# Performance work log

Hardware: AMD Instinct MI355X
Metric: run time of the kernel (lower is better)

Reference implementation:

```python
import jax, jax.numpy as jnp
import numpy as np

B, CIN, COUT, K, L = 16, 512, 512, 3, 8192
STRIDE, PAD, DIL = 1, 1, 1  # 'same' conv: Lout == L


def setup_inputs() -> dict:
    key = jax.random.key(0)
    k1, k2, k3 = jax.random.split(key, 3)
    x = jax.random.normal(k1, (B, CIN, L), dtype=jnp.float32)
    # int8 quantized weight stored as int32 for portability; values in [-128, 127]
    qweight = jax.random.randint(k2, (COUT, CIN, K), -128, 128, dtype=jnp.int32)
    scale = jnp.float32(0.01)  # per-tensor dequant scale (w_max / 127)
    bias = jax.random.normal(k3, (COUT,), dtype=jnp.float32)
    return {"x": x, "qweight": qweight, "scale": scale, "bias": bias}


def reference(x, qweight, scale, bias):
    # Dequantize: fp32 weight = int8 * scale (materialized every call, as in torch module)
    w = (qweight.astype(jnp.float32) * scale).astype(x.dtype)
    out = jax.lax.conv_general_dilated(
        x, w,
        window_strides=(STRIDE,),
        padding=[(PAD, PAD)],
        rhs_dilation=(DIL,),
        dimension_numbers=("NCH", "OIH", "NCH"),
        feature_group_count=1,
    )
    return out + bias.astype(x.dtype)[None, :, None]
```

## Files before the change

kernel.cpp:

```cpp
#include <hip/hip_runtime.h>
#include <hip/hip_bf16.h>

#define CIN   512
#define COUT  512
#define LEN   8192
#define NB    16
#define KW    3
#define PROWS 8200

#define WB_ELEMS (COUT * CIN * KW)
#define WB_BYTES ((size_t)WB_ELEMS * 2)
#define XS_BYTES ((size_t)NB * PROWS * CIN * 2)

#define BM2 256
#define BN2 256
#define BK3 64
#define NT  ((CIN / BK3) * KW)
#define TILE3 (BM2 * BK3 * 2)

typedef __attribute__((ext_vector_type(4))) float f32x4;
typedef __attribute__((ext_vector_type(8))) short bf16x8;

static __device__ __forceinline__ unsigned short f2bf(float f) {
    union { float f; unsigned u; } cv; cv.f = f;
    return (unsigned short)((cv.u + 0x7fffu + ((cv.u >> 16) & 1u)) >> 16);
}

__global__ __launch_bounds__(256) void wconv_kernel(const int* __restrict__ q,
                                                    unsigned short* __restrict__ wb) {
    int idx = blockIdx.x * 256 + threadIdx.x;
    if (idx >= WB_ELEMS) return;
    int co = idx / (KW * CIN);
    int r  = idx - co * (KW * CIN);
    int t  = r >> 9;
    int ci = r & 511;
    wb[idx] = f2bf((float)q[(co * CIN + ci) * KW + t]);
}

__global__ __launch_bounds__(256) void xprep_kernel(const float* __restrict__ x,
                                                    unsigned short* __restrict__ xs) {
    __shared__ char T[64 * 132];
    int blk = blockIdx.x;
    int b   = blk >> 10;
    int ci0 = ((blk >> 7) & 7) * 64;
    int l0  = (blk & 127) * 64;
    int tid = threadIdx.x;

    if (l0 == 0 && tid < 64)
        xs[((size_t)b * PROWS + 0) * CIN + ci0 + tid] = 0;
    if (l0 == (LEN - 64) && tid < 64)
        xs[((size_t)b * PROWS + (LEN + 1)) * CIN + ci0 + tid] = 0;

    const float* src = x + ((size_t)b * CIN + ci0) * LEN + l0;
    for (int i = tid; i < 64 * 16; i += 256) {
        int r = i >> 4, c4 = i & 15;
        f32x4 v = *(const f32x4*)(src + (size_t)r * LEN + c4 * 4);
        unsigned lo = (unsigned)f2bf(v[0]) | ((unsigned)f2bf(v[1]) << 16);
        unsigned hi = (unsigned)f2bf(v[2]) | ((unsigned)f2bf(v[3]) << 16);
        char* p = T + r * 132 + c4 * 8;
        *(unsigned*)p       = lo;
        *(unsigned*)(p + 4) = hi;
    }
    __syncthreads();
    unsigned short* dst = xs + ((size_t)b * PROWS + 1 + l0) * CIN + ci0;
    for (int i = tid; i < 64 * 8; i += 256) {
        int l = i >> 3, c8 = i & 7;
        union { bf16x8 v; unsigned short s[8]; } pk;
        #pragma unroll
        for (int j = 0; j < 8; ++j)
            pk.s[j] = *(const unsigned short*)(T + (c8 * 8 + j) * 132 + l * 2);
        *(bf16x8*)(dst + (size_t)l * CIN + c8 * 8) = pk.v;
    }
}

__global__ __launch_bounds__(512, 2) void conv_kernel(
    const unsigned short* __restrict__ xs,
    const unsigned short* __restrict__ wb,
    const float* __restrict__ scale_p,
    const float* __restrict__ bias,
    float* __restrict__ out)
{
    __shared__ char sA[2][TILE3];
    __shared__ char sB[2][TILE3];

    const int bid = blockIdx.x;
    const int logical = (bid & 7) * 128 + (bid >> 3);
    const int co_tile = logical & 1;
    const int l_tile  = logical >> 1;
    const int b   = l_tile >> 5;
    const int l0  = (l_tile & 31) * BN2;
    const int co0 = co_tile * BM2;

    const int tid  = threadIdx.x;
    const int lane = tid & 63;
    const int wid  = tid >> 6;
    const int wr   = wid >> 2;
    const int wc   = wid & 3;
    const int lhi  = lane >> 4;
    const int llo  = lane & 15;

    f32x4 acc[8][4] = {};

    const char* xsB = (const char*)(xs + ((size_t)b * PROWS + l0) * CIN);
    const char* wbB = (const char*)wb + (size_t)co0 * (KW * CIN * 2);

#define STAGEU(buf_, c_, u_) do {                                                            \
    int tap_ = (c_) % KW;  int ci0_ = ((c_) / KW) * BK3;                                     \
    int rowoff_ = ((u_) & 1) * 128;                                                          \
    const char* src0_; size_t rstride_; char* dst0_;                                         \
    if ((u_) < 2) { src0_ = xsB + ((size_t)(tap_ + rowoff_) * CIN + ci0_) * 2;               \
                    rstride_ = CIN * 2; dst0_ = &sB[buf_][rowoff_ * 128]; }                   \
    else          { src0_ = wbB + (size_t)rowoff_ * (KW * CIN * 2)                           \
                            + ((size_t)tap_ * CIN + ci0_) * 2;                               \
                    rstride_ = KW * CIN * 2; dst0_ = &sA[buf_][rowoff_ * 128]; }             \
    _Pragma("unroll")                                                                        \
    for (int kk_ = 0; kk_ < 2; ++kk_) {                                                      \
        int it_ = tid + kk_ * 512;                                                           \
        int r_ = it_ >> 3, q_ = it_ & 7;                                                     \
        __builtin_amdgcn_global_load_lds(                                                    \
            (const __attribute__((address_space(1))) unsigned int*)                          \
                (src0_ + (size_t)r_ * rstride_ + ((q_ * 16) ^ ((r_ & 7) << 4))),             \
            (__attribute__((address_space(3))) unsigned int*)(dst0_ + it_ * 16),             \
            16, 0, 0);                                                                       \
    } } while (0)

#define LDA(d_, buf_, mq_, k_) do { int row_ = (mq_) * 32 + wr * 16 + llo;                   \
    d_ = *(const bf16x8*)(&sA[buf_][0] + row_ * 128                                          \
                          + (((k_) * 64 + lhi * 16) ^ ((row_ & 7) << 4))); } while (0)
#define LDB(d_, buf_, n_, k_) do { int row_ = wc * 64 + (n_) * 16 + llo;                     \
    d_ = *(const bf16x8*)(&sB[buf_][0] + row_ * 128                                          \
                          + (((k_) * 64 + lhi * 16) ^ ((row_ & 7) << 4))); } while (0)

#define MFMA16(p_) do {                                                                      \
    __builtin_amdgcn_s_setprio(1);                                                           \
    acc[2*(p_)  ][0] = __builtin_amdgcn_mfma_f32_16x16x32_bf16(a0_, bB00, acc[2*(p_)  ][0],0,0,0); \
    acc[2*(p_)  ][1] = __builtin_amdgcn_mfma_f32_16x16x32_bf16(a0_, bB10, acc[2*(p_)  ][1],0,0,0); \
    acc[2*(p_)  ][2] = __builtin_amdgcn_mfma_f32_16x16x32_bf16(a0_, bB20, acc[2*(p_)  ][2],0,0,0); \
    acc[2*(p_)  ][3] = __builtin_amdgcn_mfma_f32_16x16x32_bf16(a0_, bB30, acc[2*(p_)  ][3],0,0,0); \
    acc[2*(p_)+1][0] = __builtin_amdgcn_mfma_f32_16x16x32_bf16(a2_, bB00, acc[2*(p_)+1][0],0,0,0); \
    acc[2*(p_)+1][1] = __builtin_amdgcn_mfma_f32_16x16x32_bf16(a2_, bB10, acc[2*(p_)+1][1],0,0,0); \
    acc[2*(p_)+1][2] = __builtin_amdgcn_mfma_f32_16x16x32_bf16(a2_, bB20, acc[2*(p_)+1][2],0,0,0); \
    acc[2*(p_)+1][3] = __builtin_amdgcn_mfma_f32_16x16x32_bf16(a2_, bB30, acc[2*(p_)+1][3],0,0,0); \
    acc[2*(p_)  ][0] = __builtin_amdgcn_mfma_f32_16x16x32_bf16(a1_, bB01, acc[2*(p_)  ][0],0,0,0); \
    acc[2*(p_)  ][1] = __builtin_amdgcn_mfma_f32_16x16x32_bf16(a1_, bB11, acc[2*(p_)  ][1],0,0,0); \
    acc[2*(p_)  ][2] = __builtin_amdgcn_mfma_f32_16x16x32_bf16(a1_, bB21, acc[2*(p_)  ][2],0,0,0); \
    acc[2*(p_)  ][3] = __builtin_amdgcn_mfma_f32_16x16x32_bf16(a1_, bB31, acc[2*(p_)  ][3],0,0,0); \
    acc[2*(p_)+1][0] = __builtin_amdgcn_mfma_f32_16x16x32_bf16(a3_, bB01, acc[2*(p_)+1][0],0,0,0); \
    acc[2*(p_)+1][1] = __builtin_amdgcn_mfma_f32_16x16x32_bf16(a3_, bB11, acc[2*(p_)+1][1],0,0,0); \
    acc[2*(p_)+1][2] = __builtin_amdgcn_mfma_f32_16x16x32_bf16(a3_, bB21, acc[2*(p_)+1][2],0,0,0); \
    acc[2*(p_)+1][3] = __builtin_amdgcn_mfma_f32_16x16x32_bf16(a3_, bB31, acc[2*(p_)+1][3],0,0,0); \
    __builtin_amdgcn_s_setprio(0);                                                           \
    } while (0)

#define BAR()    __builtin_amdgcn_s_barrier()
#define SCHED0() __builtin_amdgcn_sched_barrier(0)
#define LGKM0()  asm volatile("s_waitcnt lgkmcnt(0)" ::: "memory")

    STAGEU(0, 0, 0); STAGEU(0, 0, 1); STAGEU(0, 0, 2); STAGEU(0, 0, 3);
    asm volatile("s_waitcnt vmcnt(2)" ::: "memory");
    BAR();

    bf16x8 bB00, bB01, bB10, bB11, bB20, bB21, bB30, bB31;
    bf16x8 a0_, a1_, a2_, a3_;

    #pragma unroll 1
    for (int c = 0; c < NT - 1; ++c) {
        const int buf = c & 1, nb = buf ^ 1;
        SCHED0();
        LDB(bB00, buf, 0, 0); LDB(bB01, buf, 0, 1);
        LDB(bB10, buf, 1, 0); LDB(bB11, buf, 1, 1);
        LDB(bB20, buf, 2, 0); LDB(bB21, buf, 2, 1);
        LDB(bB30, buf, 3, 0); LDB(bB31, buf, 3, 1);
        LDA(a0_, buf, 0, 0); LDA(a1_, buf, 0, 1); LDA(a2_, buf, 1, 0); LDA(a3_, buf, 1, 1);
        STAGEU(nb, c + 1, 0);
        BAR(); LGKM0(); SCHED0();
        MFMA16(0);
        SCHED0();
        LDA(a0_, buf, 2, 0); LDA(a1_, buf, 2, 1); LDA(a2_, buf, 3, 0); LDA(a3_, buf, 3, 1);
        STAGEU(nb, c + 1, 1);
        asm volatile("s_waitcnt vmcnt(4)" ::: "memory");
        BAR(); LGKM0(); SCHED0();
        MFMA16(1);
        SCHED0();
        LDA(a0_, buf, 4, 0); LDA(a1_, buf, 4, 1); LDA(a2_, buf, 5, 0); LDA(a3_, buf, 5, 1);
        STAGEU(nb, c + 1, 2);
        BAR(); LGKM0(); SCHED0();
        MFMA16(2);
        SCHED0();
        LDA(a0_, buf, 6, 0); LDA(a1_, buf, 6, 1); LDA(a2_, buf, 7, 0); LDA(a3_, buf, 7, 1);
        STAGEU(nb, c + 1, 3);
        asm volatile("s_waitcnt vmcnt(2)" ::: "memory");
        BAR(); LGKM0(); SCHED0();
        MFMA16(3);
    }
    {
        const int buf = (NT - 1) & 1;
        SCHED0();
        LDB(bB00, buf, 0, 0); LDB(bB01, buf, 0, 1);
        LDB(bB10, buf, 1, 0); LDB(bB11, buf, 1, 1);
        LDB(bB20, buf, 2, 0); LDB(bB21, buf, 2, 1);
        LDB(bB30, buf, 3, 0); LDB(bB31, buf, 3, 1);
        LDA(a0_, buf, 0, 0); LDA(a1_, buf, 0, 1); LDA(a2_, buf, 1, 0); LDA(a3_, buf, 1, 1);
        BAR(); LGKM0(); SCHED0();
        MFMA16(0);
        SCHED0();
        LDA(a0_, buf, 2, 0); LDA(a1_, buf, 2, 1); LDA(a2_, buf, 3, 0); LDA(a3_, buf, 3, 1);
        asm volatile("s_waitcnt vmcnt(0)" ::: "memory");
        BAR(); LGKM0(); SCHED0();
        MFMA16(1);
        SCHED0();
        LDA(a0_, buf, 4, 0); LDA(a1_, buf, 4, 1); LDA(a2_, buf, 5, 0); LDA(a3_, buf, 5, 1);
        BAR(); LGKM0(); SCHED0();
        MFMA16(2);
        SCHED0();
        LDA(a0_, buf, 6, 0); LDA(a1_, buf, 6, 1); LDA(a2_, buf, 7, 0); LDA(a3_, buf, 7, 1);
        LGKM0(); SCHED0();
        MFMA16(3);
    }
#undef STAGEU
#undef LDA
#undef LDB
#undef MFMA16

    const float sc = scale_p[0];
    #pragma unroll
    for (int m = 0; m < 8; ++m) {
        #pragma unroll
        for (int j = 0; j < 4; ++j) {
            int co = co0 + m * 32 + wr * 16 + lhi * 4 + j;
            float bv = bias[co];
            size_t orow = ((size_t)b * COUT + co) * LEN + l0 + wc * 64;
            #pragma unroll
            for (int n = 0; n < 4; ++n)
                out[orow + n * 16 + llo] = sc * acc[m][n][j] + bv;
        }
    }
}

__global__ __launch_bounds__(256, 2) void conv_fb_kernel(
    const float* __restrict__ x,
    const unsigned short* __restrict__ wb,
    const float* __restrict__ scale_p,
    const float* __restrict__ bias,
    float* __restrict__ out)
{
    __shared__ char xT[132 * 128];
    const int bid = blockIdx.x;
    const int logical = (bid & 7) * 512 + (bid >> 3);
    const int co_tile = logical & 3;
    const int n_tile  = logical >> 2;
    const int b   = n_tile >> 6;
    const int l0  = (n_tile & 63) * 128;
    const int co0 = co_tile * 128;
    const int tid  = threadIdx.x;
    const int lane = tid & 63;
    const int wid  = tid >> 6;
    const int wr = wid >> 1, wc = wid & 1;
    const int lhi = lane >> 4;
    const int llo = lane & 15;
    f32x4 acc[4][4] = {};
    const float* xb = x + (size_t)b * CIN * LEN;

    for (int ci0 = 0; ci0 < CIN; ci0 += 64) {
        __syncthreads();
        for (int it = tid; it < 132 * 8; it += 256) {
            int c = it % 132;
            int o = it / 132;
            int l = l0 - 1 + c;
            float v[8];
            if (l >= 0 && l < LEN) {
                const float* src = xb + (size_t)(ci0 + o * 8) * LEN + l;
                #pragma unroll
                for (int j = 0; j < 8; ++j) v[j] = src[(size_t)j * LEN];
            } else {
                #pragma unroll
                for (int j = 0; j < 8; ++j) v[j] = 0.f;
            }
            union { bf16x8 v8; unsigned short s[8]; } pk;
            #pragma unroll
            for (int j = 0; j < 8; ++j) pk.s[j] = f2bf(v[j]);
            int byte = c * 128 + ((o * 16) ^ ((c & 7) << 4));
            *reinterpret_cast<bf16x8*>(xT + byte) = pk.v8;
        }
        __syncthreads();
        #pragma unroll
        for (int t = 0; t < KW; ++t) {
            #pragma unroll
            for (int s = 0; s < 2; ++s) {
                bf16x8 af[4];
                #pragma unroll
                for (int m = 0; m < 4; ++m)
                    af[m] = *reinterpret_cast<const bf16x8*>(
                        wb + (size_t)(co0 + wr * 64 + m * 16 + llo) * (KW * CIN)
                           + t * CIN + ci0 + s * 32 + 8 * lhi);
                bf16x8 bfr[4];
                #pragma unroll
                for (int n = 0; n < 4; ++n) {
                    int col = wc * 64 + n * 16 + llo + t;
                    int byte = col * 128 + (((s * 32 + 8 * lhi) * 2) ^ ((col & 7) << 4));
                    bfr[n] = *reinterpret_cast<const bf16x8*>(xT + byte);
                }
                #pragma unroll
                for (int m = 0; m < 4; ++m)
                    #pragma unroll
                    for (int n = 0; n < 4; ++n)
                        acc[m][n] = __builtin_amdgcn_mfma_f32_16x16x32_bf16(af[m], bfr[n], acc[m][n], 0, 0, 0);
            }
        }
    }
    const float sc = scale_p[0];
    #pragma unroll
    for (int m = 0; m < 4; ++m) {
        #pragma unroll
        for (int j = 0; j < 4; ++j) {
            int co = co0 + wr * 64 + m * 16 + lhi * 4 + j;
            float bv = bias[co];
            size_t orow = ((size_t)b * COUT + co) * LEN + l0 + wc * 64;
            #pragma unroll
            for (int n = 0; n < 4; ++n)
                out[orow + n * 16 + llo] = sc * acc[m][n][j] + bv;
        }
    }
}

extern "C" void kernel_launch(void* const* d_in, const int* in_sizes, int n_in,
                              void* d_out, int out_size, void* d_ws, size_t ws_size,
                              hipStream_t stream) {
    const float* x    = (const float*)d_in[0];
    const int*   qw   = (const int*)d_in[1];
    const float* sc   = (const float*)d_in[2];
    const float* bias = (const float*)d_in[3];
    float* out = (float*)d_out;
    unsigned short* wb = (unsigned short*)d_ws;

    wconv_kernel<<<(WB_ELEMS + 255) / 256, 256, 0, stream>>>(qw, wb);

    if (ws_size >= WB_BYTES + XS_BYTES) {
        unsigned short* xsw = (unsigned short*)((char*)d_ws + WB_BYTES);
        xprep_kernel<<<NB * 8 * (LEN / 64), 256, 0, stream>>>(x, xsw);
        conv_kernel<<<(COUT / BM2) * (NB * LEN / BN2), 512, 0, stream>>>(xsw, wb, sc, bias, out);
    } else {
        conv_fb_kernel<<<4096, 256, 0, stream>>>(x, wb, sc, bias, out);
    }
}
```

Before: 290.5 us.

## Switch conv GEMM to 32x32x16 MFMA and fuse weight/input prep kernels

Replaces the 16x16x32 bf16 MFMA tiling in the main conv kernel with 32x32x16 MFMA. This halves the MFMA instruction count per tile and changes the LDS fragment reads and epilogue indexing to match. It also merges the weight-conversion kernel into the input-prep kernel as extra blocks, saving one launch. The new accumulator layout changes output store patterns and register pressure.

Result: slower. 296.4 us (+2.0%).

```diff
diff --git a/kernel.cpp b/kernel.cpp
--- a/kernel.cpp
+++ b/kernel.cpp
@@ -12,39 +12,47 @@
 #define WB_BYTES ((size_t)WB_ELEMS * 2)
 #define XS_BYTES ((size_t)NB * PROWS * CIN * 2)
 
+#define XPREP_BLOCKS (NB * 8 * (LEN / 64))
+#define WCONV_BLOCKS ((WB_ELEMS + 255) / 256)
+
 #define BM2 256
 #define BN2 256
 #define BK3 64
-#define NT  ((CIN / BK3) * KW)
+#define NT  24
 #define TILE3 (BM2 * BK3 * 2)
 
-typedef __attribute__((ext_vector_type(4))) float f32x4;
-typedef __attribute__((ext_vector_type(8))) short bf16x8;
+typedef __attribute__((ext_vector_type(4)))  float f32x4;
+typedef __attribute__((ext_vector_type(16))) float f32x16;
+typedef __attribute__((ext_vector_type(8)))  short bf16x8;
 
 static __device__ __forceinline__ unsigned short f2bf(float f) {
     union { float f; unsigned u; } cv; cv.f = f;
     return (unsigned short)((cv.u + 0x7fffu + ((cv.u >> 16) & 1u)) >> 16);
 }
 
-__global__ __launch_bounds__(256) void wconv_kernel(const int* __restrict__ q,
-                                                    unsigned short* __restrict__ wb) {
-    int idx = blockIdx.x * 256 + threadIdx.x;
-    if (idx >= WB_ELEMS) return;
-    int co = idx / (KW * CIN);
-    int r  = idx - co * (KW * CIN);
-    int t  = r >> 9;
-    int ci = r & 511;
-    wb[idx] = f2bf((float)q[(co * CIN + ci) * KW + t]);
-}
-
-__global__ __launch_bounds__(256) void xprep_kernel(const float* __restrict__ x,
-                                                    unsigned short* __restrict__ xs) {
+__global__ __launch_bounds__(256) void prep_kernel(const float* __restrict__ x,
+                                                   const int* __restrict__ q,
+                                                   unsigned short* __restrict__ xs,
+                                                   unsigned short* __restrict__ wb) {
     __shared__ char T[64 * 132];
     int blk = blockIdx.x;
+    int tid = threadIdx.x;
+
+    if (blk >= XPREP_BLOCKS) {
+        int idx = (blk - XPREP_BLOCKS) * 256 + tid;
+        if (idx < WB_ELEMS) {
+            int co = idx / (KW * CIN);
+            int r  = idx - co * (KW * CIN);
+            int t  = r >> 9;
+            int ci = r & 511;
+            wb[idx] = f2bf((float)q[(co * CIN + ci) * KW + t]);
+        }
+        return;
+    }
+
     int b   = blk >> 10;
     int ci0 = ((blk >> 7) & 7) * 64;
     int l0  = (blk & 127) * 64;
-    int tid = threadIdx.x;
 
     if (l0 == 0 && tid < 64)
         xs[((size_t)b * PROWS + 0) * CIN + ci0 + tid] = 0;
@@ -96,10 +104,10 @@
     const int wid  = tid >> 6;
     const int wr   = wid >> 2;
     const int wc   = wid & 3;
-    const int lhi  = lane >> 4;
-    const int llo  = lane & 15;
-
-    f32x4 acc[8][4] = {};
+    const int la   = lane & 31;
+    const int lh   = lane >> 5;
+
+    f32x16 acc[4][2] = {};
 
     const char* xsB = (const char*)(xs + ((size_t)b * PROWS + l0) * CIN);
     const char* wbB = (const char*)wb + (size_t)co0 * (KW * CIN * 2);
@@ -124,31 +132,23 @@
             16, 0, 0);                                                                       \
     } } while (0)
 
-#define LDA(d_, buf_, mq_, k_) do { int row_ = (mq_) * 32 + wr * 16 + llo;                   \
+#define LDA(d_, buf_, mb_, s_) do { int row_ = (mb_) * 64 + wr * 32 + la;                    \
     d_ = *(const bf16x8*)(&sA[buf_][0] + row_ * 128                                          \
-                          + (((k_) * 64 + lhi * 16) ^ ((row_ & 7) << 4))); } while (0)
-#define LDB(d_, buf_, n_, k_) do { int row_ = wc * 64 + (n_) * 16 + llo;                     \
+                          + (((s_) * 32 + lh * 16) ^ ((row_ & 7) << 4))); } while (0)
+#define LDB(d_, buf_, nb_, s_) do { int row_ = wc * 64 + (nb_) * 32 + la;                    \
     d_ = *(const bf16x8*)(&sB[buf_][0] + row_ * 128                                          \
-                          + (((k_) * 64 + lhi * 16) ^ ((row_ & 7) << 4))); } while (0)
-
-#define MFMA16(p_) do {                                                                      \
+                          + (((s_) * 32 + lh * 16) ^ ((row_ & 7) << 4))); } while (0)
+
+#define MFMA8(MB_, B00_, B01_, B10_, B11_) do {                                              \
     __builtin_amdgcn_s_setprio(1);                                                           \
-    acc[2*(p_)  ][0] = __builtin_amdgcn_mfma_f32_16x16x32_bf16(a0_, bB00, acc[2*(p_)  ][0],0,0,0); \
-    acc[2*(p_)  ][1] = __builtin_amdgcn_mfma_f32_16x16x32_bf16(a0_, bB10, acc[2*(p_)  ][1],0,0,0); \
-    acc[2*(p_)  ][2] = __builtin_amdgcn_mfma_f32_16x16x32_bf16(a0_, bB20, acc[2*(p_)  ][2],0,0,0); \
-    acc[2*(p_)  ][3] = __builtin_amdgcn_mfma_f32_16x16x32_bf16(a0_, bB30, acc[2*(p_)  ][3],0,0,0); \
-    acc[2*(p_)+1][0] = __builtin_amdgcn_mfma_f32_16x16x32_bf16(a2_, bB00, acc[2*(p_)+1][0],0,0,0); \
-    acc[2*(p_)+1][1] = __builtin_amdgcn_mfma_f32_16x16x32_bf16(a2_, bB10, acc[2*(p_)+1][1],0,0,0); \
-    acc[2*(p_)+1][2] = __builtin_amdgcn_mfma_f32_16x16x32_bf16(a2_, bB20, acc[2*(p_)+1][2],0,0,0); \
-    acc[2*(p_)+1][3] = __builtin_amdgcn_mfma_f32_16x16x32_bf16(a2_, bB30, acc[2*(p_)+1][3],0,0,0); \
-    acc[2*(p_)  ][0] = __builtin_amdgcn_mfma_f32_16x16x32_bf16(a1_, bB01, acc[2*(p_)  ][0],0,0,0); \
-    acc[2*(p_)  ][1] = __builtin_amdgcn_mfma_f32_16x16x32_bf16(a1_, bB11, acc[2*(p_)  ][1],0,0,0); \
-    acc[2*(p_)  ][2] = __builtin_amdgcn_mfma_f32_16x16x32_bf16(a1_, bB21, acc[2*(p_)  ][2],0,0,0); \
-    acc[2*(p_)  ][3] = __builtin_amdgcn_mfma_f32_16x16x32_bf16(a1_, bB31, acc[2*(p_)  ][3],0,0,0); \
-    acc[2*(p_)+1][0] = __builtin_amdgcn_mfma_f32_16x16x32_bf16(a3_, bB01, acc[2*(p_)+1][0],0,0,0); \
-    acc[2*(p_)+1][1] = __builtin_amdgcn_mfma_f32_16x16x32_bf16(a3_, bB11, acc[2*(p_)+1][1],0,0,0); \
-    acc[2*(p_)+1][2] = __builtin_amdgcn_mfma_f32_16x16x32_bf16(a3_, bB21, acc[2*(p_)+1][2],0,0,0); \
-    acc[2*(p_)+1][3] = __builtin_amdgcn_mfma_f32_16x16x32_bf16(a3_, bB31, acc[2*(p_)+1][3],0,0,0); \
+    acc[(MB_)  ][0] = __builtin_amdgcn_mfma_f32_32x32x16_bf16(a0_, B00_, acc[(MB_)  ][0],0,0,0); \
+    acc[(MB_)  ][1] = __builtin_amdgcn_mfma_f32_32x32x16_bf16(a0_, B01_, acc[(MB_)  ][1],0,0,0); \
+    acc[(MB_)+1][0] = __builtin_amdgcn_mfma_f32_32x32x16_bf16(a2_, B00_, acc[(MB_)+1][0],0,0,0); \
+    acc[(MB_)+1][1] = __builtin_amdgcn_mfma_f32_32x32x16_bf16(a2_, B01_, acc[(MB_)+1][1],0,0,0); \
+    acc[(MB_)  ][0] = __builtin_amdgcn_mfma_f32_32x32x16_bf16(a1_, B10_, acc[(MB_)  ][0],0,0,0); \
+    acc[(MB_)  ][1] = __builtin_amdgcn_mfma_f32_32x32x16_bf16(a1_, B11_, acc[(MB_)  ][1],0,0,0); \
+    acc[(MB_)+1][0] = __builtin_amdgcn_mfma_f32_32x32x16_bf16(a3_, B10_, acc[(MB_)+1][0],0,0,0); \
+    acc[(MB_)+1][1] = __builtin_amdgcn_mfma_f32_32x32x16_bf16(a3_, B11_, acc[(MB_)+1][1],0,0,0); \
     __builtin_amdgcn_s_setprio(0);                                                           \
     } while (0)
 
@@ -160,81 +160,92 @@
     asm volatile("s_waitcnt vmcnt(2)" ::: "memory");
     BAR();
 
-    bf16x8 bB00, bB01, bB10, bB11, bB20, bB21, bB30, bB31;
+    bf16x8 b00, b01, b10, b11, b20, b21, b30, b31;
     bf16x8 a0_, a1_, a2_, a3_;
 
     #pragma unroll 1
     for (int c = 0; c < NT - 1; ++c) {
         const int buf = c & 1, nb = buf ^ 1;
         SCHED0();
-        LDB(bB00, buf, 0, 0); LDB(bB01, buf, 0, 1);
-        LDB(bB10, buf, 1, 0); LDB(bB11, buf, 1, 1);
-        LDB(bB20, buf, 2, 0); LDB(bB21, buf, 2, 1);
-        LDB(bB30, buf, 3, 0); LDB(bB31, buf, 3, 1);
+        LDB(b00, buf, 0, 0); LDB(b01, buf, 1, 0);
+        LDB(b10, buf, 0, 1); LDB(b11, buf, 1, 1);
+        LDB(b20, buf, 0, 2); LDB(b21, buf, 1, 2);
+        LDB(b30, buf, 0, 3); LDB(b31, buf, 1, 3);
         LDA(a0_, buf, 0, 0); LDA(a1_, buf, 0, 1); LDA(a2_, buf, 1, 0); LDA(a3_, buf, 1, 1);
         STAGEU(nb, c + 1, 0);
         BAR(); LGKM0(); SCHED0();
-        MFMA16(0);
-        SCHED0();
-        LDA(a0_, buf, 2, 0); LDA(a1_, buf, 2, 1); LDA(a2_, buf, 3, 0); LDA(a3_, buf, 3, 1);
+        MFMA8(0, b00, b01, b10, b11);
+        SCHED0();
+        LDA(a0_, buf, 0, 2); LDA(a1_, buf, 0, 3); LDA(a2_, buf, 1, 2); LDA(a3_, buf, 1, 3);
         STAGEU(nb, c + 1, 1);
         asm volatile("s_waitcnt vmcnt(4)" ::: "memory");
         BAR(); LGKM0(); SCHED0();
-        MFMA16(1);
-        SCHED0();
-        LDA(a0_, buf, 4, 0); LDA(a1_, buf, 4, 1); LDA(a2_, buf, 5, 0); LDA(a3_, buf, 5, 1);
+        MFMA8(0, b20, b21, b30, b31);
+        SCHED0();
+        LDA(a0_, buf, 2, 0); LDA(a1_, buf, 2, 1); LDA(a2_, buf, 3, 0); LDA(a3_, buf, 3, 1);
         STAGEU(nb, c + 1, 2);
         BAR(); LGKM0(); SCHED0();
-        MFMA16(2);
-        SCHED0();
-        LDA(a0_, buf, 6, 0); LDA(a1_, buf, 6, 1); LDA(a2_, buf, 7, 0); LDA(a3_, buf, 7, 1);
+        MFMA8(2, b00, b01, b10, b11);
+        SCHED0();
+        LDA(a0_, buf, 2, 2); LDA(a1_, buf, 2, 3); LDA(a2_, buf, 3, 2); LDA(a3_, buf, 3, 3);
         STAGEU(nb, c + 1, 3);
         asm volatile("s_waitcnt vmcnt(2)" ::: "memory");
         BAR(); LGKM0(); SCHED0();
-        MFMA16(3);
+        MFMA8(2, b20, b21, b30, b31);
     }
     {
         const int buf = (NT - 1) & 1;
         SCHED0();
-        LDB(bB00, buf, 0, 0); LDB(bB01, buf, 0, 1);
-        LDB(bB10, buf, 1, 0); LDB(bB11, buf, 1, 1);
-        LDB(bB20, buf, 2, 0); LDB(bB21, buf, 2, 1);
-        LDB(bB30, buf, 3, 0); LDB(bB31, buf, 3, 1);
+        LDB(b00, buf, 0, 0); LDB(b01, buf, 1, 0);
+        LDB(b10, buf, 0, 1); LDB(b11, buf, 1, 1);
+        LDB(b20, buf, 0, 2); LDB(b21, buf, 1, 2);
+        LDB(b30, buf, 0, 3); LDB(b31, buf, 1, 3);
         LDA(a0_, buf, 0, 0); LDA(a1_, buf, 0, 1); LDA(a2_, buf, 1, 0); LDA(a3_, buf, 1, 1);
         BAR(); LGKM0(); SCHED0();
-        MFMA16(0);
+        MFMA8(0, b00, b01, b10, b11);
+        SCHED0();
+        LDA(a0_, buf, 0, 2); LDA(a1_, buf, 0, 3); LDA(a2_, buf, 1, 2); LDA(a3_, buf, 1, 3);
+        asm volatile("s_waitcnt vmcnt(0)" ::: "memory");
+        BAR(); LGKM0(); SCHED0();
+        MFMA8(0, b20, b21, b30, b31);
         SCHED0();
         LDA(a0_, buf, 2, 0); LDA(a1_, buf, 2, 1); LDA(a2_, buf, 3, 0); LDA(a3_, buf, 3, 1);
-        asm volatile("s_waitcnt vmcnt(0)" ::: "memory");
-        BAR(); LGKM0(); SCHED0();
-        MFMA16(1);
-        SCHED0();
-        LDA(a0_, buf, 4, 0); LDA(a1_, buf, 4, 1); LDA(a2_, buf, 5, 0); LDA(a3_, buf, 5, 1);
-        BAR(); LGKM0(); SCHED0();
-        MFMA16(2);
-        SCHED0();
-        LDA(a0_, buf, 6, 0); LDA(a1_, buf, 6, 1); LDA(a2_, buf, 7, 0); LDA(a3_, buf, 7, 1);
+        BAR(); LGKM0(); SCHED0();
+        MFMA8(2, b00, b01, b10, b11);
+        SCHED0();
+        LDA(a0_, buf, 2, 2); LDA(a1_, buf, 2, 3); LDA(a2_, buf, 3, 2); LDA(a3_, buf, 3, 3);
         LGKM0(); SCHED0();
-        MFMA16(3);
+        MFMA8(2, b20, b21, b30, b31);
     }
 #undef STAGEU
 #undef LDA
 #undef LDB
-#undef MFMA16
+#undef MFMA8
 
     const float sc = scale_p[0];
     #pragma unroll
-    for (int m = 0; m < 8; ++m) {
+    for (int mb = 0; mb < 4; ++mb) {
+        const int coB = co0 + mb * 64 + wr * 32 + 4 * lh;
         #pragma unroll
-        for (int j = 0; j < 4; ++j) {
-            int co = co0 + m * 32 + wr * 16 + lhi * 4 + j;
+        for (int rg = 0; rg < 16; ++rg) {
+            int co = coB + (rg & 3) + 8 * (rg >> 2);
             float bv = bias[co];
-            size_t orow = ((size_t)b * COUT + co) * LEN + l0 + wc * 64;
-            #pragma unroll
-            for (int n = 0; n < 4; ++n)
-                out[orow + n * 16 + llo] = sc * acc[m][n][j] + bv;
-        }
-    }
+            size_t orow = ((size_t)b * COUT + co) * LEN + l0 + wc * 64 + la;
+            out[orow]      = sc * acc[mb][0][rg] + bv;
+            out[orow + 32] = sc * acc[mb][1][rg] + bv;
+        }
+    }
+}
+
+__global__ __launch_bounds__(256) void wconv_kernel(const int* __restrict__ q,
+                                                    unsigned short* __restrict__ wb) {
+    int idx = blockIdx.x * 256 + threadIdx.x;
+    if (idx >= WB_ELEMS) return;
+    int co = idx / (KW * CIN);
+    int r  = idx - co * (KW * CIN);
+    int t  = r >> 9;
+    int ci = r & 511;
+    wb[idx] = f2bf((float)q[(co * CIN + ci) * KW + t]);
 }
 
 __global__ __launch_bounds__(256, 2) void conv_fb_kernel(
@@ -333,13 +344,12 @@
     float* out = (float*)d_out;
     unsigned short* wb = (unsigned short*)d_ws;
 
-    wconv_kernel<<<(WB_ELEMS + 255) / 256, 256, 0, stream>>>(qw, wb);
-
     if (ws_size >= WB_BYTES + XS_BYTES) {
         unsigned short* xsw = (unsigned short*)((char*)d_ws + WB_BYTES);
-        xprep_kernel<<<NB * 8 * (LEN / 64), 256, 0, stream>>>(x, xsw);
+        prep_kernel<<<XPREP_BLOCKS + WCONV_BLOCKS, 256, 0, stream>>>(x, qw, xsw, wb);
         conv_kernel<<<(COUT / BM2) * (NB * LEN / BN2), 512, 0, stream>>>(xsw, wb, sc, bias, out);
     } else {
+        wconv_kernel<<<WCONV_BLOCKS, 256, 0, stream>>>(qw, wb);
         conv_fb_kernel<<<4096, 256, 0, stream>>>(x, wb, sc, bias, out);
     }
 }
```
